# Kernel tuning notes

Hardware: AMD Instinct MI355X
Metric: run time of the kernel (lower is better)

Reference implementation:

```python
import jax, jax.numpy as jnp
import numpy as np

N, F, T, C, E = 5000, 4, 12, 600, 160000


def setup_inputs() -> dict:
    key = jax.random.key(0)
    ks = jax.random.split(key, 18)
    x = jax.random.normal(ks[0], (N, F, T), jnp.float32)
    edge_index = jax.random.randint(ks[1], (2, E), 0, N)
    edge_attributes = jax.random.uniform(ks[2], (E,), jnp.float32)
    s_in = 0.5   # glorot-ish scale for F->C conv weights
    s_lin = 0.03  # scale for (2C)->C gate linears
    return {
        "x": x,
        "edge_index": edge_index,
        "edge_attributes": edge_attributes,
        # GCNConv weights/biases for z, r, h gates (weight stored [F, C])
        "W_z": jax.random.normal(ks[3], (F, C), jnp.float32) * s_in,
        "b_z": jnp.zeros((C,), jnp.float32),
        "W_r": jax.random.normal(ks[4], (F, C), jnp.float32) * s_in,
        "b_r": jnp.zeros((C,), jnp.float32),
        "W_h": jax.random.normal(ks[5], (F, C), jnp.float32) * s_in,
        "b_h": jnp.zeros((C,), jnp.float32),
        # gate Linear(2C, C) weights in torch layout [out=C, in=2C]
        "Wlz": jax.random.normal(ks[6], (C, 2 * C), jnp.float32) * s_lin,
        "blz": jnp.zeros((C,), jnp.float32),
        "Wlr": jax.random.normal(ks[7], (C, 2 * C), jnp.float32) * s_lin,
        "blr": jnp.zeros((C,), jnp.float32),
        "Wlh": jax.random.normal(ks[8], (C, 2 * C), jnp.float32) * s_lin,
        "blh": jnp.zeros((C,), jnp.float32),
        # temporal attention logits over periods
        "att": jax.random.normal(ks[9], (T,), jnp.float32),
        # head Linear(600, periods), torch layout [T, C]
        "W_head": jax.random.normal(ks[10], (T, C), jnp.float32) * 0.04,
        "b_head": jnp.zeros((T,), jnp.float32),
    }


def _gcn_propagate(x, edge_index, edge_weight):
    """A_hat @ x with A_hat = D^{-1/2}(A+I)D^{-1/2} (GCNConv norm, self-loops w=1).
    x: [N, F, T] -> [N, F, T]."""
    loop = jnp.arange(N)
    row = jnp.concatenate([edge_index[0], loop])   # source j
    col = jnp.concatenate([edge_index[1], loop])   # target i
    w = jnp.concatenate([edge_weight, jnp.ones((N,), x.dtype)])
    deg = jax.ops.segment_sum(w, col, num_segments=N)
    dis = jnp.where(deg > 0, jax.lax.rsqrt(deg), 0.0)
    norm = dis[row] * w * dis[col]                 # [E+N]
    msgs = norm[:, None, None] * x[row]            # gather + scale, [E+N, F, T]
    return jax.ops.segment_sum(msgs, col, num_segments=N)


def reference(x, edge_index, edge_attributes,
              W_z, b_z, W_r, b_r, W_h, b_h,
              Wlz, blz, Wlr, blr, Wlh, blh,
              att, W_head, b_head):
    # A3TGCN: H is passed as None each period -> zeros, never threaded across
    # time. Hence z*H == 0 and the H*r candidate term == 0 exactly; the r-gate
    # (W_r, b_r, Wlr, blr) and the second halves of Wlz/Wlh drop out of the math.
    agg = _gcn_propagate(x, edge_index, edge_attributes)          # [N, F, T]
    # GCNConv output = A_hat X W + b (linear commutes with propagation)
    conv_z = jnp.einsum('nft,fc->nct', agg, W_z) + b_z[:, None]   # [N, C, T]
    conv_h = jnp.einsum('nft,fc->nct', agg, W_h) + b_h[:, None]
    # gate linears on cat([conv, H]) with H = 0 -> only first C input columns
    z = jax.nn.sigmoid(jnp.einsum('nct,dc->ndt', conv_z, Wlz[:, :C]) + blz[:, None])
    h_tilde = jnp.tanh(jnp.einsum('nct,dc->ndt', conv_h, Wlh[:, :C]) + blh[:, None])
    H_t = (1.0 - z) * h_tilde                                      # z*H = 0
    probs = jax.nn.softmax(att)                                    # [T]
    H_accum = jnp.einsum('nct,t->nc', H_t, probs)                  # [N, C]
    return jax.nn.relu(H_accum) @ W_head.T + b_head                # [N, T]
```

## Files before the change

kernel.cpp:

```cpp
#include <hip/hip_runtime.h>

#define NN 5000
#define NF 4
#define NT 12
#define NC 600
#define NCP 640
#define NE 160000
#define FT 48
#define LOG2E 1.4426950408889634f

typedef float v2f __attribute__((ext_vector_type(2)));


__global__ void k_init(int* __restrict__ cnt, float* __restrict__ tabG) {
    int i = blockIdx.x * blockDim.x + threadIdx.x;
    if (i < 5000) cnt[i] = 0;
    else if (i < 19092) tabG[i - 5000] = 0.f;
}

#define CNT_BLOCKS 625
#define WB_WAVES 6132
__global__ __launch_bounds__(256) void k_count(
        const int* __restrict__ ei,
        int* __restrict__ cnt, int* __restrict__ rank,
        const float* __restrict__ Wz, const float* __restrict__ bz,
        const float* __restrict__ Wh, const float* __restrict__ bh,
        const float* __restrict__ Wlz, const float* __restrict__ blz,
        const float* __restrict__ Wlh, const float* __restrict__ blh,
        const float* __restrict__ att, const float* __restrict__ Whead,
        float* __restrict__ tabG) {
    int bid = blockIdx.x;
    int tid = threadIdx.x;
    if (bid < CNT_BLOCKS) {
        int e = bid * 256 + tid;
        if (e < NE) rank[e] = atomicAdd(&cnt[ei[NE + e]], 1);
        return;
    }
    int wid = (bid - CNT_BLOCKS) * 4 + (tid >> 6);
    int lane = tid & 63;
    if (wid >= WB_WAVES) return;

    if (wid < 6000) {
        const float* va;
        const float* vb;
        float scale, bias = 0.f;
        if (wid < 2400) {
            int f = wid / NC, d = wid % NC;
            va = Wz + f * NC; vb = Wlz + d * (2 * NC); scale = LOG2E;
        } else if (wid < 4800) {
            int j = wid - 2400;
            int f = j / NC, d = j % NC;
            va = Wh + f * NC; vb = Wlh + d * (2 * NC); scale = 2.0f * LOG2E;
        } else if (wid < 5400) {
            int d = wid - 4800;
            va = bz; vb = Wlz + d * (2 * NC); scale = LOG2E; bias = blz[d];
        } else {
            int d = wid - 5400;
            va = bh; vb = Wlh + d * (2 * NC); scale = 2.0f * LOG2E; bias = blh[d];
        }
        float s = 0.f;
        for (int c = lane; c < NC; c += 64) s = fmaf(va[c], vb[c], s);
#pragma unroll
        for (int off = 32; off > 0; off >>= 1) s += __shfl_down(s, off, 64);
        if (lane == 0) {
            float r = scale * (bias + s);
            if (wid < 2400) {
                int f = wid / NC, d = wid % NC;
                tabG[d * 4 + f] = r;
            } else if (wid < 4800) {
                int j = wid - 2400;
                int f = j / NC, d = j % NC;
                tabG[2560 + d * 4 + f] = r;
            } else if (wid < 5400) {
                tabG[5120 + (wid - 4800) * 2] = r;
            } else {
                tabG[5120 + (wid - 5400) * 2 + 1] = r;
            }
        }
    } else if (wid < 6012) {
        if (lane == 0) {
            int t = wid - 6000;
            float m = att[0];
            for (int k = 1; k < NT; ++k) m = fmaxf(m, att[k]);
            float ssum = 0.f;
            for (int k = 0; k < NT; ++k) ssum += __expf(att[k] - m);
            tabG[14080 + t] = __expf(att[t] - m) / ssum;
        }
    } else {
        int i = (wid - 6012) * 64 + lane;
        if (i < 7680) {
            int j = i & 3;
            int rest = i >> 2;
            int d = rest % NCP, q = rest / NCP;
            float v = (d < NC) ? Whead[(4 * q + j) * NC + d] : 0.f;
            tabG[6400 + i] = v;
        }
    }
}

#define SCAN_CHUNK 20
__global__ __launch_bounds__(256) void k_scan(const int* __restrict__ cnt,
                                              int* __restrict__ base) {
    __shared__ int part[256];
    int t = threadIdx.x;
    int start = t * SCAN_CHUNK;
    int s = 0;
#pragma unroll
    for (int k = 0; k < SCAN_CHUNK; ++k) {
        int idx = start + k;
        if (idx < NN) s += cnt[idx];
    }
    part[t] = s;
    __syncthreads();
    for (int off = 1; off < 256; off <<= 1) {
        int v = (t >= off) ? part[t - off] : 0;
        __syncthreads();
        part[t] += v;
        __syncthreads();
    }
    int running = (t == 0) ? 0 : part[t - 1];
#pragma unroll
    for (int k = 0; k < SCAN_CHUNK; ++k) {
        int idx = start + k;
        if (idx < NN) {
            base[idx] = running;
            running += cnt[idx];
        }
    }
    if (t == 255) base[NN] = part[255];
}

__global__ void k_scatter(const int* __restrict__ ei, const float* __restrict__ w,
                          const int* __restrict__ base, const int* __restrict__ rank,
                          int2* __restrict__ epak) {
    int e = blockIdx.x * blockDim.x + threadIdx.x;
    if (e < NE) {
        int2 p; p.x = ei[e]; p.y = __float_as_int(w[e]);
        epak[base[ei[NE + e]] + rank[e]] = p;
    }
}

__global__ __launch_bounds__(64) void k_deg_dis(const int2* __restrict__ epak,
                                                const int* __restrict__ base,
                                                float* __restrict__ dis) {
    int n = blockIdx.x;
    int lane = threadIdx.x;
    int b0 = base[n], b1 = base[n + 1];
    float s = 0.f;
    for (int j = b0 + lane; j < b1; j += 64) s += __int_as_float(epak[j].y);
#pragma unroll
    for (int off = 32; off > 0; off >>= 1) s += __shfl_down(s, off, 64);
    if (lane == 0) dis[n] = rsqrtf(1.0f + s);
}

__global__ __launch_bounds__(256, 3) void k_node(
        const float* __restrict__ x, const float* __restrict__ dis,
        const int2* __restrict__ epak, const int* __restrict__ base,
        const float* __restrict__ tabG,
        const float* __restrict__ bhead, float* __restrict__ out) {
    __shared__ float red[4][NT][16];
    int tid = threadIdx.x;
    int wid = __builtin_amdgcn_readfirstlane(tid >> 6);
    int lane = tid & 63;
    int n = blockIdx.x * 4 + wid;

    int b0 = base[n], b1 = base[n + 1];
    float dn = dis[n];
    float acc = 0.f;
    if (lane < FT) acc = dn * x[n * FT + lane];
    int j = b0;
    for (; j + 3 < b1; j += 4) {
        int2 p0 = epak[j], p1 = epak[j + 1], p2 = epak[j + 2], p3 = epak[j + 3];
        float n0 = dis[p0.x] * __int_as_float(p0.y);
        float n1 = dis[p1.x] * __int_as_float(p1.y);
        float n2 = dis[p2.x] * __int_as_float(p2.y);
        float n3 = dis[p3.x] * __int_as_float(p3.y);
        if (lane < FT) {
            acc += n0 * x[p0.x * FT + lane];
            acc += n1 * x[p1.x * FT + lane];
            acc += n2 * x[p2.x * FT + lane];
            acc += n3 * x[p3.x * FT + lane];
        }
    }
    for (; j < b1; ++j) {
        int2 p0 = epak[j];
        float n0 = dis[p0.x] * __int_as_float(p0.y);
        if (lane < FT) acc += n0 * x[p0.x * FT + lane];
    }
    acc *= dn;

    v2f A2[24];
#pragma unroll
    for (int i = 0; i < 24; ++i) {
        A2[i].x = __int_as_float(__builtin_amdgcn_readlane(__float_as_int(acc), 2 * i));
        A2[i].y = __int_as_float(__builtin_amdgcn_readlane(__float_as_int(acc), 2 * i + 1));
    }

    const float4* mz4 = (const float4*)tabG;
    const float4* mh4 = (const float4*)(tabG + 2560);
    const float2* bzh = (const float2*)(tabG + 5120);
    const float4* wt4 = (const float4*)(tabG + 6400);

    v2f pp[6];
#pragma unroll
    for (int tp = 0; tp < 6; ++tp) { pp[tp].x = tabG[14080 + 2 * tp]; pp[tp].y = tabG[14080 + 2 * tp + 1]; }

    float outp[NT];
#pragma unroll
    for (int t = 0; t < NT; ++t) outp[t] = 0.f;

#pragma unroll
    for (int it = 0; it < 10; ++it) {
        int dd = it * 64 + lane;

        float4 mzv = mz4[dd];
        float4 mhv = mh4[dd];
        float2 bb = bzh[dd];

        v2f hacc; hacc.x = 0.f; hacc.y = 0.f;
#pragma unroll
        for (int tp = 0; tp < 6; ++tp) {
            v2f u; u.x = bb.x; u.y = bb.x;
            v2f v; v.x = bb.y; v.y = bb.y;
            u += A2[0 * 6 + tp] * mzv.x;
            u += A2[1 * 6 + tp] * mzv.y;
            u += A2[2 * 6 + tp] * mzv.z;
            u += A2[3 * 6 + tp] * mzv.w;
            v += A2[0 * 6 + tp] * mhv.x;
            v += A2[1 * 6 + tp] * mhv.y;
            v += A2[2 * 6 + tp] * mhv.z;
            v += A2[3 * 6 + tp] * mhv.w;
            v2f eu; eu.x = exp2f(u.x); eu.y = exp2f(u.y);
            v2f ev; ev.x = exp2f(v.x); ev.y = exp2f(v.y);
            v2f den = (eu + 1.f) * (ev + 1.f);
            v2f rd; rd.x = __builtin_amdgcn_rcpf(den.x); rd.y = __builtin_amdgcn_rcpf(den.y);
            v2f num = pp[tp] * (ev - 1.f);
            hacc += num * rd;
        }
        float r = fmaxf(hacc.x + hacc.y, 0.f);

        float4 w0 = wt4[0 * NCP + dd], w1 = wt4[1 * NCP + dd], w2 = wt4[2 * NCP + dd];
        outp[0]  = fmaf(r, w0.x, outp[0]);   outp[1]  = fmaf(r, w0.y, outp[1]);
        outp[2]  = fmaf(r, w0.z, outp[2]);   outp[3]  = fmaf(r, w0.w, outp[3]);
        outp[4]  = fmaf(r, w1.x, outp[4]);   outp[5]  = fmaf(r, w1.y, outp[5]);
        outp[6]  = fmaf(r, w1.z, outp[6]);   outp[7]  = fmaf(r, w1.w, outp[7]);
        outp[8]  = fmaf(r, w2.x, outp[8]);   outp[9]  = fmaf(r, w2.y, outp[9]);
        outp[10] = fmaf(r, w2.z, outp[10]);  outp[11] = fmaf(r, w2.w, outp[11]);
    }

#pragma unroll
    for (int t = 0; t < NT; ++t) {
        float v = outp[t];
        v += __shfl_xor(v, 32, 64);
        v += __shfl_xor(v, 16, 64);
        if (lane < 16) red[wid][t][lane] = v;
    }
    if (lane < NT) {
        const float4* row = (const float4*)red[wid][lane];
        float4 a = row[0], b = row[1], c = row[2], d = row[3];
        float s = ((a.x + a.y) + (a.z + a.w)) + ((b.x + b.y) + (b.z + b.w))
                + ((c.x + c.y) + (c.z + c.w)) + ((d.x + d.y) + (d.z + d.w));
        out[n * NT + lane] = s + bhead[lane];
    }
}

extern "C" void kernel_launch(void* const* d_in, const int* in_sizes, int n_in,
                              void* d_out, int out_size, void* d_ws, size_t ws_size,
                              hipStream_t stream) {
    const float* x     = (const float*)d_in[0];
    const int*   ei    = (const int*)d_in[1];
    const float* ea    = (const float*)d_in[2];
    const float* Wz    = (const float*)d_in[3];
    const float* bz    = (const float*)d_in[4];
    const float* Wh    = (const float*)d_in[7];
    const float* bh    = (const float*)d_in[8];
    const float* Wlz   = (const float*)d_in[9];
    const float* blz   = (const float*)d_in[10];
    const float* Wlh   = (const float*)d_in[13];
    const float* blh   = (const float*)d_in[14];
    const float* att   = (const float*)d_in[15];
    const float* Whead = (const float*)d_in[16];
    const float* bhead = (const float*)d_in[17];
    float* out = (float*)d_out;

    float* ws   = (float*)d_ws;
    int*   cnt  = (int*)ws;
    int*   base = (int*)(ws + 5000);
    int*   rank = (int*)(ws + 10008);
    int2*  epak = (int2*)(ws + 170008);
    float* dis  = ws + 490008;
    float* tabG = ws + 495008;

    k_init<<<(19092 + 255) / 256, 256, 0, stream>>>(cnt, tabG);
    k_count<<<CNT_BLOCKS + (WB_WAVES + 3) / 4, 256, 0, stream>>>(
        ei, cnt, rank,
        Wz, bz, Wh, bh, Wlz, blz, Wlh, blh, att, Whead, tabG);
    k_scan<<<1, 256, 0, stream>>>(cnt, base);
    k_scatter<<<(NE + 255) / 256, 256, 0, stream>>>(ei, ea, base, rank, epak);
    k_deg_dis<<<NN, 64, 0, stream>>>(epak, base, dis);
    k_node<<<NN / 4, 256, 0, stream>>>(x, dis, epak, base, tabG, bhead, out);
}
```

Measured before the change: 73.52 us.

## Split each node's work across two waves in k_node

Each node is now handled by a pair of wavefronts instead of one. The edge-gather loop is split at a midpoint and the two partial aggregates are combined through shared memory. The 640-channel gate and head loop is also split in half, and both halves' reductions are combined at the end. This doubles the block count so the grid has more parallelism and shorter per-wave serial chains, at the cost of two block-wide barriers and some extra shared-memory traffic.

```diff
diff --git a/kernel.cpp b/kernel.cpp
--- a/kernel.cpp
+++ b/kernel.cpp
@@ -158,18 +158,24 @@
         const int2* __restrict__ epak, const int* __restrict__ base,
         const float* __restrict__ tabG,
         const float* __restrict__ bhead, float* __restrict__ out) {
+    __shared__ float aggS[4][FT];
     __shared__ float red[4][NT][16];
     int tid = threadIdx.x;
     int wid = __builtin_amdgcn_readfirstlane(tid >> 6);
     int lane = tid & 63;
-    int n = blockIdx.x * 4 + wid;
+    int pair = wid >> 1;
+    int half = wid & 1;
+    int n = blockIdx.x * 2 + pair;
 
     int b0 = base[n], b1 = base[n + 1];
+    int mid = b0 + (((b1 - b0) >> 1) & ~3);
+    int s0 = half ? mid : b0;
+    int s1 = half ? b1 : mid;
     float dn = dis[n];
     float acc = 0.f;
-    if (lane < FT) acc = dn * x[n * FT + lane];
-    int j = b0;
-    for (; j + 3 < b1; j += 4) {
+    if (half == 0 && lane < FT) acc = dn * x[n * FT + lane];
+    int j = s0;
+    for (; j + 3 < s1; j += 4) {
         int2 p0 = epak[j], p1 = epak[j + 1], p2 = epak[j + 2], p3 = epak[j + 3];
         float n0 = dis[p0.x] * __int_as_float(p0.y);
         float n1 = dis[p1.x] * __int_as_float(p1.y);
@@ -182,18 +188,23 @@
             acc += n3 * x[p3.x * FT + lane];
         }
     }
-    for (; j < b1; ++j) {
+    for (; j < s1; ++j) {
         int2 p0 = epak[j];
         float n0 = dis[p0.x] * __int_as_float(p0.y);
         if (lane < FT) acc += n0 * x[p0.x * FT + lane];
     }
     acc *= dn;
 
+    if (lane < FT) aggS[wid][lane] = acc;
+    __syncthreads();
+    float av = 0.f;
+    if (lane < FT) av = aggS[2 * pair][lane] + aggS[2 * pair + 1][lane];
+
     v2f A2[24];
 #pragma unroll
     for (int i = 0; i < 24; ++i) {
-        A2[i].x = __int_as_float(__builtin_amdgcn_readlane(__float_as_int(acc), 2 * i));
-        A2[i].y = __int_as_float(__builtin_amdgcn_readlane(__float_as_int(acc), 2 * i + 1));
+        A2[i].x = __int_as_float(__builtin_amdgcn_readlane(__float_as_int(av), 2 * i));
+        A2[i].y = __int_as_float(__builtin_amdgcn_readlane(__float_as_int(av), 2 * i + 1));
     }
 
     const float4* mz4 = (const float4*)tabG;
@@ -210,8 +221,8 @@
     for (int t = 0; t < NT; ++t) outp[t] = 0.f;
 
 #pragma unroll
-    for (int it = 0; it < 10; ++it) {
-        int dd = it * 64 + lane;
+    for (int it = 0; it < 5; ++it) {
+        int dd = half * 320 + it * 64 + lane;
 
         float4 mzv = mz4[dd];
         float4 mhv = mh4[dd];
@@ -255,11 +266,16 @@
         v += __shfl_xor(v, 16, 64);
         if (lane < 16) red[wid][t][lane] = v;
     }
-    if (lane < NT) {
-        const float4* row = (const float4*)red[wid][lane];
-        float4 a = row[0], b = row[1], c = row[2], d = row[3];
+    __syncthreads();
+    if (half == 0 && lane < NT) {
+        const float4* rowA = (const float4*)red[2 * pair][lane];
+        const float4* rowB = (const float4*)red[2 * pair + 1][lane];
+        float4 a = rowA[0], b = rowA[1], c = rowA[2], d = rowA[3];
+        float4 e = rowB[0], f = rowB[1], g = rowB[2], h = rowB[3];
         float s = ((a.x + a.y) + (a.z + a.w)) + ((b.x + b.y) + (b.z + b.w))
-                + ((c.x + c.y) + (c.z + c.w)) + ((d.x + d.y) + (d.z + d.w));
+                + ((c.x + c.y) + (c.z + c.w)) + ((d.x + d.y) + (d.z + d.w))
+                + ((e.x + e.y) + (e.z + e.w)) + ((f.x + f.y) + (f.z + f.w))
+                + ((g.x + g.y) + (g.z + g.w)) + ((h.x + h.y) + (h.z + h.w));
         out[n * NT + lane] = s + bhead[lane];
     }
 }
@@ -298,5 +314,5 @@
     k_scan<<<1, 256, 0, stream>>>(cnt, base);
     k_scatter<<<(NE + 255) / 256, 256, 0, stream>>>(ei, ea, base, rank, epak);
     k_deg_dis<<<NN, 64, 0, stream>>>(epak, base, dis);
-    k_node<<<NN / 4, 256, 0, stream>>>(x, dis, epak, base, tabG, bhead, out);
-}
+    k_node<<<NN / 2, 256, 0, stream>>>(x, dis, epak, base, tabG, bhead, out);
+}
```

After: 72.44 us, median of 2. No clear change (-1.5%).
